# Performance work log

Measured on AMD Instinct MI355X. Metric: run time of the kernel, lower is better.

Reference implementation:

```python
import jax, jax.numpy as jnp
import numpy as np

N = 100000      # num nodes
E = 1600000     # num edges (avg degree 16)
D_IN = 128
D_OUT = 128
HOPS = 2


def setup_inputs() -> dict:
    key = jax.random.key(0)
    k1, k2, k3, k4, k5 = jax.random.split(key, 5)
    x = jax.random.normal(k1, (N, D_IN), dtype=jnp.float32)
    edge_index = jax.random.randint(k2, (2, E), 0, N, dtype=jnp.int32)
    edge_weight = jax.random.uniform(k3, (E,), dtype=jnp.float32)
    weight = jax.random.normal(k4, (D_OUT, D_IN), dtype=jnp.float32) * 0.05
    bias = jax.random.normal(k5, (D_OUT,), dtype=jnp.float32) * 0.05
    return {"x": x, "edge_index": edge_index, "edge_weight": edge_weight,
            "weight": weight, "bias": bias}


def reference(x, edge_index, edge_weight, weight, bias):
    # --- gcn_norm: add self-loops (fill value 1) and symmetric normalization ---
    row, col = edge_index[0], edge_index[1]            # source, target
    loop = jnp.arange(N, dtype=row.dtype)
    row = jnp.concatenate([row, loop])
    col = jnp.concatenate([col, loop])
    ew = jnp.concatenate([edge_weight, jnp.ones((N,), x.dtype)])
    deg = jax.ops.segment_sum(ew, col, num_segments=N)  # in-degree at targets
    dinv = jnp.where(deg > 0, jax.lax.rsqrt(deg), 0.0)
    norm = dinv[row] * ew * dinv[col]                   # [E+N]
    # --- K-hop propagation: h <- A_hat @ h ---
    h = x
    for _ in range(HOPS):
        h = jax.ops.segment_sum(norm[:, None] * h[row], col, num_segments=N)
    # --- final linear ---
    return h @ weight.T + bias
```

## Files before the change

### kernel.cpp

```cpp
#include <hip/hip_runtime.h>


constexpr int D = 128;

__global__ void zero_u64(unsigned long long* p, int n) {
    int i = blockIdx.x * blockDim.x + threadIdx.x;
    if (i < n) p[i] = 0ULL;
}

__global__ void count_packed(const int* __restrict__ col, const float* __restrict__ ew,
                             unsigned long long* __restrict__ cnt4, int N, int E) {
    int e = blockIdx.x * blockDim.x + threadIdx.x;
    if (e >= E) return;
    int c = col[e];
    unsigned long long v = (1ULL << 40) |
        (unsigned long long)(ew[e] * 4294967296.0f);
    int rep = (e >> 6) & 3;
    atomicAdd(&cnt4[(size_t)rep * N + c], v);
}

__global__ void finalize_deg(const unsigned long long* __restrict__ cnt4,
                             float* __restrict__ dinv, int* __restrict__ degi, int N) {
    int i = blockIdx.x * blockDim.x + threadIdx.x;
    if (i >= N) return;
    unsigned long long s = cnt4[i] + cnt4[(size_t)N + i] +
                           cnt4[2 * (size_t)N + i] + cnt4[3 * (size_t)N + i];
    int cnt = (int)(s >> 40);
    float deg = (float)((double)(s & ((1ULL << 40) - 1)) * (1.0 / 4294967296.0));
    dinv[i] = rsqrtf(deg + 1.0f);
    degi[i] = cnt;
}

__global__ __launch_bounds__(256) void scan_bsum(const int* __restrict__ degi,
                                                 int* __restrict__ bsum, int n) {
    int base = blockIdx.x * 1024;
    int t = threadIdx.x;
    int s = 0;
    #pragma unroll
    for (int k = 0; k < 4; ++k) { int i = base + t * 4 + k; if (i < n) s += degi[i]; }
    __shared__ int sh[256];
    sh[t] = s; __syncthreads();
    for (int off = 128; off > 0; off >>= 1) {
        if (t < off) sh[t] += sh[t + off];
        __syncthreads();
    }
    if (t == 0) bsum[blockIdx.x] = sh[0];
}

__global__ void scan_exclusive_bsum(int* bsum, int nb) {
    if (blockIdx.x == 0 && threadIdx.x == 0) {
        int run = 0;
        for (int i = 0; i < nb; ++i) { int v = bsum[i]; bsum[i] = run; run += v; }
    }
}

__global__ __launch_bounds__(256) void scan_write_rowptr(const int* __restrict__ degi,
                                                         const int* __restrict__ bsum,
                                                         int* __restrict__ rowptr, int n, int E) {
    int base = blockIdx.x * 1024;
    int t = threadIdx.x;
    int v[4]; int s = 0;
    #pragma unroll
    for (int k = 0; k < 4; ++k) { int i = base + t * 4 + k; v[k] = (i < n) ? degi[i] : 0; s += v[k]; }
    __shared__ int sh[256];
    sh[t] = s; __syncthreads();
    for (int off = 1; off < 256; off <<= 1) {
        int x = (t >= off) ? sh[t - off] : 0;
        __syncthreads();
        sh[t] += x;
        __syncthreads();
    }
    int pre = bsum[blockIdx.x] + ((t > 0) ? sh[t - 1] : 0);
    #pragma unroll
    for (int k = 0; k < 4; ++k) { int i = base + t * 4 + k; if (i < n) rowptr[i] = pre; pre += v[k]; }
    if (blockIdx.x == 0 && t == 0) rowptr[n] = E;
}

__global__ void copy_cursor(const int* __restrict__ rowptr, int* __restrict__ cursor, int n) {
    int i = blockIdx.x * blockDim.x + threadIdx.x;
    if (i < n) cursor[i] = rowptr[i];
}

__global__ void bin_kernel(const int* __restrict__ row, const int* __restrict__ col,
                           const float* __restrict__ ew, const float* __restrict__ dinv,
                           int* __restrict__ cursor,
                           int2* __restrict__ ent, int E) {
    int e = blockIdx.x * blockDim.x + threadIdx.x;
    if (e >= E) return;
    int r = row[e], c = col[e];
    int pos = atomicAdd(&cursor[c], 1);
    ent[pos] = make_int2(r, __float_as_int(dinv[r] * ew[e] * dinv[c]));
}

#define GR 8
__global__ __launch_bounds__(512) void gemm_xwT(const float* __restrict__ X,
                                                const float* __restrict__ W,
                                                float* __restrict__ Y, int nrows) {
    __shared__ float Wl[D][D + 1];
    int tid = threadIdx.x;
    for (int i = tid; i < D * D; i += 512) Wl[i >> 7][i & 127] = W[i];
    __syncthreads();
    int jg = tid & 31;
    int rg = tid >> 5;
    int row0 = blockIdx.x * 128 + rg * GR;
    const float4* X4 = reinterpret_cast<const float4*>(X);
    float acc[GR][4];
    #pragma unroll
    for (int i = 0; i < GR; ++i)
        #pragma unroll
        for (int jj = 0; jj < 4; ++jj) acc[i][jj] = 0.0f;

    bool full = (row0 + GR <= nrows);
    for (int d4 = 0; d4 < D; d4 += 4) {
        float4 xv[GR];
        if (full) {
            #pragma unroll
            for (int i = 0; i < GR; ++i)
                xv[i] = X4[((size_t)(row0 + i) * D + d4) >> 2];
        } else {
            #pragma unroll
            for (int i = 0; i < GR; ++i) {
                int r = row0 + i;
                xv[i] = (r < nrows) ? X4[((size_t)r * D + d4) >> 2]
                                    : make_float4(0.f, 0.f, 0.f, 0.f);
            }
        }
        #pragma unroll
        for (int dd = 0; dd < 4; ++dd) {
            int d = d4 + dd;
            float w[4];
            #pragma unroll
            for (int jj = 0; jj < 4; ++jj) w[jj] = Wl[jg + 32 * jj][d];
            #pragma unroll
            for (int i = 0; i < GR; ++i) {
                float xc = (dd == 0) ? xv[i].x : (dd == 1) ? xv[i].y
                         : (dd == 2) ? xv[i].z : xv[i].w;
                #pragma unroll
                for (int jj = 0; jj < 4; ++jj)
                    acc[i][jj] = fmaf(xc, w[jj], acc[i][jj]);
            }
        }
    }
    #pragma unroll
    for (int i = 0; i < GR; ++i) {
        int r = row0 + i;
        if (r < nrows) {
            #pragma unroll
            for (int jj = 0; jj < 4; ++jj)
                Y[(size_t)r * D + jg + 32 * jj] = acc[i][jj];
        }
    }
}

__global__ __launch_bounds__(256) void hop_gather_kernel(
    const int* __restrict__ rowptr, const int2* __restrict__ ent,
    const float* __restrict__ dinv, const float* __restrict__ h,
    float* __restrict__ out, const float* __restrict__ bias, int N) {
    long long t = (long long)blockIdx.x * blockDim.x + threadIdx.x;
    int node = (int)(t >> 5);
    int lane = (int)(t & 31);
    if (node >= N) return;
    int beg = rowptr[node], end = rowptr[node + 1];
    float s = dinv[node];
    float ss = s * s;
    const float4* h4 = reinterpret_cast<const float4*>(h);
    float4 v = h4[(size_t)node * 32 + lane];
    float4 acc = make_float4(ss * v.x, ss * v.y, ss * v.z, ss * v.w);
    if (bias != nullptr) {
        float4 bv = reinterpret_cast<const float4*>(bias)[lane];
        acc.x += bv.x; acc.y += bv.y; acc.z += bv.z; acc.w += bv.w;
    }
    for (int base = beg; base < end; base += 32) {
        int cnt = min(32, end - base);
        int2 e = make_int2(0, 0);
        if (lane < cnt) e = ent[base + lane];
        for (int j = 0; j < cnt; ++j) {
            int   sj = __shfl(e.x, j, 32);
            float wj = __shfl(__int_as_float(e.y), j, 32);
            float4 hv = h4[(size_t)sj * 32 + lane];
            acc.x = fmaf(wj, hv.x, acc.x);
            acc.y = fmaf(wj, hv.y, acc.y);
            acc.z = fmaf(wj, hv.z, acc.z);
            acc.w = fmaf(wj, hv.w, acc.w);
        }
    }
    reinterpret_cast<float4*>(out)[(size_t)node * 32 + lane] = acc;
}

extern "C" void kernel_launch(void* const* d_in, const int* in_sizes, int n_in,
                              void* d_out, int out_size, void* d_ws, size_t ws_size,
                              hipStream_t stream) {
    const float* x    = (const float*)d_in[0];
    const int*   eidx = (const int*)d_in[1];
    const float* ew   = (const float*)d_in[2];
    const float* W    = (const float*)d_in[3];
    const float* bias = (const float*)d_in[4];
    float* out = (float*)d_out;

    const int N = in_sizes[0] / D;
    const int E = in_sizes[2];
    const int* erow = eidx;
    const int* ecol = eidx + E;

    float* h1     = (float*)d_ws;
    unsigned long long* cnt4 = (unsigned long long*)d_ws;
    int2*  ent    = (int2*)(h1 + (size_t)N * D);
    float* dinv   = (float*)(ent + E);
    int*   degi   = (int*)(dinv + N);
    int*   cursor = degi + N;
    int*   rowptr = cursor + N;
    int*   bsum   = rowptr + N + 1;

    const int B = 256;
    const int nb_scan = (N + 1023) / 1024;

    zero_u64<<<(4 * N + B - 1) / B, B, 0, stream>>>(cnt4, 4 * N);
    count_packed<<<(E + B - 1) / B, B, 0, stream>>>(ecol, ew, cnt4, N, E);
    finalize_deg<<<(N + B - 1) / B, B, 0, stream>>>(cnt4, dinv, degi, N);

    scan_bsum<<<nb_scan, 256, 0, stream>>>(degi, bsum, N);
    scan_exclusive_bsum<<<1, 1, 0, stream>>>(bsum, nb_scan);
    scan_write_rowptr<<<nb_scan, 256, 0, stream>>>(degi, bsum, rowptr, N, E);
    copy_cursor<<<(N + B - 1) / B, B, 0, stream>>>(rowptr, cursor, N);

    bin_kernel<<<(E + B - 1) / B, B, 0, stream>>>(erow, ecol, ew, dinv, cursor, ent, E);

    gemm_xwT<<<(N + 127) / 128, 512, 0, stream>>>(x, W, out, N);

    const long long gthreads = (long long)N * 32;
    const int gblocks = (int)((gthreads + B - 1) / B);
    hop_gather_kernel<<<gblocks, B, 0, stream>>>(rowptr, ent, dinv, out, h1, nullptr, N);
    hop_gather_kernel<<<gblocks, B, 0, stream>>>(rowptr, ent, dinv, h1, out, bias, N);
}
```

Baseline: 588.9 us.

## Store intermediate features in bf16 and spread binning atomics over four replicas

The projected features and the first-hop output are now stored as bf16 and widened to fp32 in the gather kernels, halving the bytes each random neighbor-row gather reads. Accumulation stays in fp32. Separately, the degree counters are interleaved per node as four replicas, and the scan runs over all 4N slots so binning uses per-replica cursors, cutting atomic contention and dropping the cursor copy kernel. The trade-off is bf16 rounding error in the intermediate activations and a scan that is four times longer.

```diff
diff --git a/kernel.cpp b/kernel.cpp
--- a/kernel.cpp
+++ b/kernel.cpp
@@ -1,4 +1,5 @@
 #include <hip/hip_runtime.h>
+#include <hip/hip_bf16.h>
 
 
 constexpr int D = 128;
@@ -9,35 +10,33 @@
 }
 
 __global__ void count_packed(const int* __restrict__ col, const float* __restrict__ ew,
-                             unsigned long long* __restrict__ cnt4, int N, int E) {
+                             unsigned long long* __restrict__ cnt4, int E) {
     int e = blockIdx.x * blockDim.x + threadIdx.x;
     if (e >= E) return;
     int c = col[e];
     unsigned long long v = (1ULL << 40) |
         (unsigned long long)(ew[e] * 4294967296.0f);
     int rep = (e >> 6) & 3;
-    atomicAdd(&cnt4[(size_t)rep * N + c], v);
+    atomicAdd(&cnt4[(size_t)c * 4 + rep], v);
 }
 
 __global__ void finalize_deg(const unsigned long long* __restrict__ cnt4,
-                             float* __restrict__ dinv, int* __restrict__ degi, int N) {
+                             float* __restrict__ dinv, int N) {
     int i = blockIdx.x * blockDim.x + threadIdx.x;
     if (i >= N) return;
-    unsigned long long s = cnt4[i] + cnt4[(size_t)N + i] +
-                           cnt4[2 * (size_t)N + i] + cnt4[3 * (size_t)N + i];
-    int cnt = (int)(s >> 40);
+    const unsigned long long* p = cnt4 + (size_t)i * 4;
+    unsigned long long s = p[0] + p[1] + p[2] + p[3];
     float deg = (float)((double)(s & ((1ULL << 40) - 1)) * (1.0 / 4294967296.0));
     dinv[i] = rsqrtf(deg + 1.0f);
-    degi[i] = cnt;
-}
-
-__global__ __launch_bounds__(256) void scan_bsum(const int* __restrict__ degi,
+}
+
+__global__ __launch_bounds__(256) void scan_bsum(const unsigned long long* __restrict__ cnt,
                                                  int* __restrict__ bsum, int n) {
     int base = blockIdx.x * 1024;
     int t = threadIdx.x;
     int s = 0;
     #pragma unroll
-    for (int k = 0; k < 4; ++k) { int i = base + t * 4 + k; if (i < n) s += degi[i]; }
+    for (int k = 0; k < 4; ++k) { int i = base + t * 4 + k; if (i < n) s += (int)(cnt[i] >> 40); }
     __shared__ int sh[256];
     sh[t] = s; __syncthreads();
     for (int off = 128; off > 0; off >>= 1) {
@@ -54,14 +53,14 @@
     }
 }
 
-__global__ __launch_bounds__(256) void scan_write_rowptr(const int* __restrict__ degi,
+__global__ __launch_bounds__(256) void scan_write_rowptr(const unsigned long long* __restrict__ cnt,
                                                          const int* __restrict__ bsum,
-                                                         int* __restrict__ rowptr, int n, int E) {
+                                                         int* __restrict__ rowptr4, int n) {
     int base = blockIdx.x * 1024;
     int t = threadIdx.x;
     int v[4]; int s = 0;
     #pragma unroll
-    for (int k = 0; k < 4; ++k) { int i = base + t * 4 + k; v[k] = (i < n) ? degi[i] : 0; s += v[k]; }
+    for (int k = 0; k < 4; ++k) { int i = base + t * 4 + k; v[k] = (i < n) ? (int)(cnt[i] >> 40) : 0; s += v[k]; }
     __shared__ int sh[256];
     sh[t] = s; __syncthreads();
     for (int off = 1; off < 256; off <<= 1) {
@@ -72,30 +71,32 @@
     }
     int pre = bsum[blockIdx.x] + ((t > 0) ? sh[t - 1] : 0);
     #pragma unroll
-    for (int k = 0; k < 4; ++k) { int i = base + t * 4 + k; if (i < n) rowptr[i] = pre; pre += v[k]; }
-    if (blockIdx.x == 0 && t == 0) rowptr[n] = E;
-}
-
-__global__ void copy_cursor(const int* __restrict__ rowptr, int* __restrict__ cursor, int n) {
+    for (int k = 0; k < 4; ++k) { int i = base + t * 4 + k; if (i < n) rowptr4[i] = pre; pre += v[k]; }
+}
+
+__global__ void compact_rowptr(const int* __restrict__ rowptr4, int* __restrict__ rowptr,
+                               int N, int E) {
     int i = blockIdx.x * blockDim.x + threadIdx.x;
-    if (i < n) cursor[i] = rowptr[i];
+    if (i < N) rowptr[i] = rowptr4[i * 4];
+    if (i == N) rowptr[N] = E;
 }
 
 __global__ void bin_kernel(const int* __restrict__ row, const int* __restrict__ col,
                            const float* __restrict__ ew, const float* __restrict__ dinv,
-                           int* __restrict__ cursor,
+                           int* __restrict__ cursor4,
                            int2* __restrict__ ent, int E) {
     int e = blockIdx.x * blockDim.x + threadIdx.x;
     if (e >= E) return;
     int r = row[e], c = col[e];
-    int pos = atomicAdd(&cursor[c], 1);
+    int rep = (e >> 6) & 3;
+    int pos = atomicAdd(&cursor4[(size_t)c * 4 + rep], 1);
     ent[pos] = make_int2(r, __float_as_int(dinv[r] * ew[e] * dinv[c]));
 }
 
 #define GR 8
-__global__ __launch_bounds__(512) void gemm_xwT(const float* __restrict__ X,
-                                                const float* __restrict__ W,
-                                                float* __restrict__ Y, int nrows) {
+__global__ __launch_bounds__(512) void gemm_xwT_bf16(const float* __restrict__ X,
+                                                     const float* __restrict__ W,
+                                                     unsigned short* __restrict__ Yb, int nrows) {
     __shared__ float Wl[D][D + 1];
     int tid = threadIdx.x;
     for (int i = tid; i < D * D; i += 512) Wl[i >> 7][i & 127] = W[i];
@@ -146,16 +147,22 @@
         int r = row0 + i;
         if (r < nrows) {
             #pragma unroll
-            for (int jj = 0; jj < 4; ++jj)
-                Y[(size_t)r * D + jg + 32 * jj] = acc[i][jj];
-        }
-    }
-}
-
-__global__ __launch_bounds__(256) void hop_gather_kernel(
+            for (int jj = 0; jj < 4; ++jj) {
+                __hip_bfloat16 hv = __float2bfloat16(acc[i][jj]);
+                Yb[(size_t)r * D + jg + 32 * jj] = *reinterpret_cast<unsigned short*>(&hv);
+            }
+        }
+    }
+}
+
+__device__ __forceinline__ float bf_lo(unsigned int u) { return __uint_as_float(u << 16); }
+__device__ __forceinline__ float bf_hi(unsigned int u) { return __uint_as_float(u & 0xffff0000u); }
+
+__global__ __launch_bounds__(256) void hop_gather_bf16(
     const int* __restrict__ rowptr, const int2* __restrict__ ent,
-    const float* __restrict__ dinv, const float* __restrict__ h,
-    float* __restrict__ out, const float* __restrict__ bias, int N) {
+    const float* __restrict__ dinv, const unsigned short* __restrict__ h,
+    float* __restrict__ outf, unsigned short* __restrict__ outb,
+    const float* __restrict__ bias, int N) {
     long long t = (long long)blockIdx.x * blockDim.x + threadIdx.x;
     int node = (int)(t >> 5);
     int lane = (int)(t & 31);
@@ -163,9 +170,10 @@
     int beg = rowptr[node], end = rowptr[node + 1];
     float s = dinv[node];
     float ss = s * s;
-    const float4* h4 = reinterpret_cast<const float4*>(h);
-    float4 v = h4[(size_t)node * 32 + lane];
-    float4 acc = make_float4(ss * v.x, ss * v.y, ss * v.z, ss * v.w);
+    const uint2* h2 = reinterpret_cast<const uint2*>(h);
+    uint2 sv = h2[(size_t)node * 32 + lane];
+    float4 acc = make_float4(ss * bf_lo(sv.x), ss * bf_hi(sv.x),
+                             ss * bf_lo(sv.y), ss * bf_hi(sv.y));
     if (bias != nullptr) {
         float4 bv = reinterpret_cast<const float4*>(bias)[lane];
         acc.x += bv.x; acc.y += bv.y; acc.z += bv.z; acc.w += bv.w;
@@ -177,14 +185,27 @@
         for (int j = 0; j < cnt; ++j) {
             int   sj = __shfl(e.x, j, 32);
             float wj = __shfl(__int_as_float(e.y), j, 32);
-            float4 hv = h4[(size_t)sj * 32 + lane];
-            acc.x = fmaf(wj, hv.x, acc.x);
-            acc.y = fmaf(wj, hv.y, acc.y);
-            acc.z = fmaf(wj, hv.z, acc.z);
-            acc.w = fmaf(wj, hv.w, acc.w);
-        }
-    }
-    reinterpret_cast<float4*>(out)[(size_t)node * 32 + lane] = acc;
+            uint2 hv = h2[(size_t)sj * 32 + lane];
+            acc.x = fmaf(wj, bf_lo(hv.x), acc.x);
+            acc.y = fmaf(wj, bf_hi(hv.x), acc.y);
+            acc.z = fmaf(wj, bf_lo(hv.y), acc.z);
+            acc.w = fmaf(wj, bf_hi(hv.y), acc.w);
+        }
+    }
+    if (outf != nullptr) {
+        reinterpret_cast<float4*>(outf)[(size_t)node * 32 + lane] = acc;
+    } else {
+        __hip_bfloat16 b0 = __float2bfloat16(acc.x);
+        __hip_bfloat16 b1 = __float2bfloat16(acc.y);
+        __hip_bfloat16 b2 = __float2bfloat16(acc.z);
+        __hip_bfloat16 b3 = __float2bfloat16(acc.w);
+        uint2 pk;
+        pk.x = (unsigned int)*reinterpret_cast<unsigned short*>(&b0) |
+               ((unsigned int)*reinterpret_cast<unsigned short*>(&b1) << 16);
+        pk.y = (unsigned int)*reinterpret_cast<unsigned short*>(&b2) |
+               ((unsigned int)*reinterpret_cast<unsigned short*>(&b3) << 16);
+        reinterpret_cast<uint2*>(outb)[(size_t)node * 32 + lane] = pk;
+    }
 }
 
 extern "C" void kernel_launch(void* const* d_in, const int* in_sizes, int n_in,
@@ -202,33 +223,37 @@
     const int* erow = eidx;
     const int* ecol = eidx + E;
 
-    float* h1     = (float*)d_ws;
-    unsigned long long* cnt4 = (unsigned long long*)d_ws;
-    int2*  ent    = (int2*)(h1 + (size_t)N * D);
+    unsigned int* yb  = (unsigned int*)d_ws;
+    unsigned int* h1b = yb + (size_t)N * 64;
+    int2*  ent    = (int2*)(h1b + (size_t)N * 64);
     float* dinv   = (float*)(ent + E);
-    int*   degi   = (int*)(dinv + N);
-    int*   cursor = degi + N;
-    int*   rowptr = cursor + N;
-    int*   bsum   = rowptr + N + 1;
+    int*   rowptr = (int*)(dinv + N);
+
+    unsigned long long* cnt4 = (unsigned long long*)yb;
+    int* rowptr4 = (int*)h1b;
+    int* bsum    = rowptr4 + 4 * N + 4;
 
     const int B = 256;
-    const int nb_scan = (N + 1023) / 1024;
-
-    zero_u64<<<(4 * N + B - 1) / B, B, 0, stream>>>(cnt4, 4 * N);
-    count_packed<<<(E + B - 1) / B, B, 0, stream>>>(ecol, ew, cnt4, N, E);
-    finalize_deg<<<(N + B - 1) / B, B, 0, stream>>>(cnt4, dinv, degi, N);
-
-    scan_bsum<<<nb_scan, 256, 0, stream>>>(degi, bsum, N);
+    const int M = 4 * N;
+    const int nb_scan = (M + 1023) / 1024;
+
+    zero_u64<<<(M + B - 1) / B, B, 0, stream>>>(cnt4, M);
+    count_packed<<<(E + B - 1) / B, B, 0, stream>>>(ecol, ew, cnt4, E);
+    finalize_deg<<<(N + B - 1) / B, B, 0, stream>>>(cnt4, dinv, N);
+
+    scan_bsum<<<nb_scan, 256, 0, stream>>>(cnt4, bsum, M);
     scan_exclusive_bsum<<<1, 1, 0, stream>>>(bsum, nb_scan);
-    scan_write_rowptr<<<nb_scan, 256, 0, stream>>>(degi, bsum, rowptr, N, E);
-    copy_cursor<<<(N + B - 1) / B, B, 0, stream>>>(rowptr, cursor, N);
-
-    bin_kernel<<<(E + B - 1) / B, B, 0, stream>>>(erow, ecol, ew, dinv, cursor, ent, E);
-
-    gemm_xwT<<<(N + 127) / 128, 512, 0, stream>>>(x, W, out, N);
+    scan_write_rowptr<<<nb_scan, 256, 0, stream>>>(cnt4, bsum, rowptr4, M);
+    compact_rowptr<<<(N + 1 + B - 1) / B, B, 0, stream>>>(rowptr4, rowptr, N, E);
+
+    bin_kernel<<<(E + B - 1) / B, B, 0, stream>>>(erow, ecol, ew, dinv, rowptr4, ent, E);
+
+    gemm_xwT_bf16<<<(N + 127) / 128, 512, 0, stream>>>(x, W, (unsigned short*)yb, N);
 
     const long long gthreads = (long long)N * 32;
     const int gblocks = (int)((gthreads + B - 1) / B);
-    hop_gather_kernel<<<gblocks, B, 0, stream>>>(rowptr, ent, dinv, out, h1, nullptr, N);
-    hop_gather_kernel<<<gblocks, B, 0, stream>>>(rowptr, ent, dinv, h1, out, bias, N);
-}
+    hop_gather_bf16<<<gblocks, B, 0, stream>>>(rowptr, ent, dinv, (unsigned short*)yb,
+                                               nullptr, (unsigned short*)h1b, nullptr, N);
+    hop_gather_bf16<<<gblocks, B, 0, stream>>>(rowptr, ent, dinv, (unsigned short*)h1b,
+                                               out, nullptr, bias, N);
+}
```

Measured after the change: 517.7 us. 12.1% less time.
